# Kernel tuning notes

Hardware: AMD Instinct MI355X
Metric: run time of the kernel (lower is better)

## Reference

```python
import jax, jax.numpy as jnp
import numpy as np

N = 100000      # nodes
R = 3           # relations
E = 1600000     # edges per relation
IN, HID, OUT = 128, 128, 64


def setup_inputs() -> dict:
    key = jax.random.key(0)
    ks = jax.random.split(key, 16)
    x = jax.random.normal(ks[0], (N, IN), dtype=jnp.float32)
    src = jax.random.randint(ks[1], (R, E), 0, N, dtype=jnp.int32)
    dst = jax.random.randint(ks[2], (R, E), 0, N, dtype=jnp.int32)
    dims = [(IN, HID), (HID, HID), (HID, HID), (HID, HID), (HID, HID), (HID, OUT)]
    inp = {"x": x, "src": src, "dst": dst}
    for i, (di, do) in enumerate(dims):
        w = jax.random.normal(ks[3 + i], (R, di, do), dtype=jnp.float32) / np.sqrt(di).astype(np.float32)
        inp[f"W{i+1}"] = w
        inp[f"b{i+1}"] = jnp.zeros((R, do), dtype=jnp.float32)
    return inp


def _degree_norms(src, dst):
    # GraphConv norm='both': scale by out-deg(src)^-1/2 before, in-deg(dst)^-1/2 after
    ones = jnp.ones((E,), dtype=jnp.float32)
    inv_out, inv_in = [], []
    for r in range(R):
        d_out = jax.ops.segment_sum(ones, src[r], num_segments=N)
        d_in = jax.ops.segment_sum(ones, dst[r], num_segments=N)
        inv_out.append(jax.lax.rsqrt(jnp.maximum(d_out, 1.0))[:, None])
        inv_in.append(jax.lax.rsqrt(jnp.maximum(d_in, 1.0))[:, None])
    return inv_out, inv_in


def _hetero_conv(h, W, b, src, dst, inv_out, inv_in):
    # sum over relations of GraphConv_r(h): D_dst^-1/2 A_r (D_src^-1/2 h) W_r + b_r
    out = None
    for r in range(R):
        m = (h * inv_out[r]) @ W[r]                      # [N, do], weight-first (same math)
        agg = jax.ops.segment_sum(m[src[r]], dst[r], num_segments=N)
        term = agg * inv_in[r] + b[r]
        out = term if out is None else out + term
    return out


def reference(x, src, dst, W1, b1, W2, b2, W3, b3, W4, b4, W5, b5, W6, b6):
    inv_out, inv_in = _degree_norms(src, dst)
    h = x
    for W, b in [(W1, b1), (W2, b2), (W3, b3), (W4, b4), (W5, b5)]:
        h = jax.nn.relu(_hetero_conv(h, W, b, src, dst, inv_out, inv_in))
    return _hetero_conv(h, W6, b6, src, dst, inv_out, inv_in)
```

## Files before the change

kernel.cpp:

```cpp
#include <hip/hip_runtime.h>
#include <hip/hip_bf16.h>
#include <hip/hip_fp16.h>

constexpr int N_NODES = 100000;
constexpr int N_REL   = 3;
constexpr int N_EDGE  = 1600000;
constexpr int NCHUNK  = (N_NODES + 1023) / 1024;

constexpr int CCHUNK = 50;
constexpr int CH     = N_EDGE / CCHUNK;
constexpr int SUBN   = 50000;
constexpr int WPP    = SUBN / 4;
constexpr int CWORDS = N_NODES / 4;

constexpr int BSH  = 7;
constexpr int BNPB = 1 << BSH;
constexpr int NB   = (N_NODES + BNPB - 1) / BNPB;

typedef __attribute__((ext_vector_type(8))) short short8;
typedef __attribute__((ext_vector_type(4))) float f32x4;

__device__ inline ushort f2bf(float x) {
  unsigned u = __float_as_uint(x);
  unsigned r = u + 0x7FFFu + ((u >> 16) & 1u);
  return (ushort)(r >> 16);
}
__device__ inline float bf2f(ushort h) { return __uint_as_float(((unsigned)h) << 16); }


__global__ __launch_bounds__(1024)
void count_kernel(const int* __restrict__ src, const int* __restrict__ dst,
                  uint* __restrict__ part) {
  int c = blockIdx.x, r = blockIdx.y, dir = blockIdx.z;
  const int* ids = (dir ? dst : src) + (size_t)r * N_EDGE + (size_t)c * CH;
  uint* p = part + ((size_t)(c * N_REL + r) * 2 + dir) * CWORDS;
  __shared__ uint hist[WPP];
  #pragma unroll
  for (int pass = 0; pass < 2; pass++) {
    int base = pass * SUBN;
    for (int i = threadIdx.x; i < WPP; i += 1024) hist[i] = 0u;
    __syncthreads();
    for (int e = (int)threadIdx.x; e < CH; e += 1024) {
      int ln = ids[e] - base;
      if ((unsigned)ln < (unsigned)SUBN)
        atomicAdd(&hist[ln >> 2], 1u << ((ln & 3) * 8));
    }
    __syncthreads();
    for (int i = threadIdx.x; i < WPP; i += 1024) p[pass * WPP + i] = hist[i];
    __syncthreads();
  }
}

__global__ void reduce_kernel(const uint* __restrict__ part,
                              int* __restrict__ deg_out, int* __restrict__ deg_in) {
  int i = blockIdx.x * 256 + threadIdx.x;
  if (i >= N_REL * CWORDS) return;
  int r = i / CWORDS, w = i % CWORDS;
  uint aoe = 0, aoo = 0, aie = 0, aio = 0;
  for (int c = 0; c < CCHUNK; c++) {
    uint vo = part[((size_t)(c * N_REL + r) * 2 + 0) * CWORDS + w];
    uint vi = part[((size_t)(c * N_REL + r) * 2 + 1) * CWORDS + w];
    aoe += vo & 0x00FF00FFu; aoo += (vo >> 8) & 0x00FF00FFu;
    aie += vi & 0x00FF00FFu; aio += (vi >> 8) & 0x00FF00FFu;
  }
  int4 dout = make_int4((int)(aoe & 0xFFFFu), (int)(aoo & 0xFFFFu),
                        (int)(aoe >> 16),     (int)(aoo >> 16));
  int4 din  = make_int4((int)(aie & 0xFFFFu), (int)(aio & 0xFFFFu),
                        (int)(aie >> 16),     (int)(aio >> 16));
  *(int4*)&deg_out[(size_t)r * N_NODES + w * 4] = dout;
  *(int4*)&deg_in [(size_t)r * N_NODES + w * 4] = din;
}

__global__ void inv_kernel(const int* __restrict__ deg_out, const int* __restrict__ deg_in,
                           float* __restrict__ inv_out, float* __restrict__ inv_in) {
  int i = blockIdx.x * blockDim.x + threadIdx.x;
  if (i >= N_REL * N_NODES) return;
  inv_out[i] = rsqrtf(fmaxf((float)deg_out[i], 1.0f));
  inv_in[i]  = rsqrtf(fmaxf((float)deg_in[i],  1.0f));
}

__global__ void scan1_kernel(const int* __restrict__ deg_in, int* __restrict__ excl,
                             int* __restrict__ part) {
  int r = blockIdx.y;
  int i = blockIdx.x * 1024 + threadIdx.x;
  int v = (i < N_NODES) ? deg_in[r * N_NODES + i] : 0;
  __shared__ int sm[1024];
  sm[threadIdx.x] = v;
  __syncthreads();
  for (int off = 1; off < 1024; off <<= 1) {
    int t = (threadIdx.x >= (unsigned)off) ? sm[threadIdx.x - off] : 0;
    __syncthreads();
    sm[threadIdx.x] += t;
    __syncthreads();
  }
  if (i < N_NODES) excl[r * N_NODES + i] = sm[threadIdx.x] - v;
  if (threadIdx.x == 1023) part[r * NCHUNK + blockIdx.x] = sm[1023];
}

__global__ void scan2_kernel(int* __restrict__ part) {
  int r = blockIdx.x;
  int* p = part + r * NCHUNK;
  __shared__ int sm[128];
  int tid = threadIdx.x;
  int v = (tid < NCHUNK) ? p[tid] : 0;
  sm[tid] = v;
  __syncthreads();
  for (int off = 1; off < 128; off <<= 1) {
    int t = (tid >= off) ? sm[tid - off] : 0;
    __syncthreads();
    sm[tid] += t;
    __syncthreads();
  }
  if (tid < NCHUNK) p[tid] = sm[tid] - v;
}

__global__ void scan3_kernel(const int* __restrict__ excl, const int* __restrict__ part,
                             int* __restrict__ row_off) {
  int r = blockIdx.y;
  int i = blockIdx.x * 1024 + threadIdx.x;
  if (i < N_NODES) row_off[r * (N_NODES + 1) + i] = excl[r * N_NODES + i] + part[r * NCHUNK + (i >> 10)];
  if (i == N_NODES) row_off[r * (N_NODES + 1) + N_NODES] = N_EDGE;
}


__global__ __launch_bounds__(64)
void boff_kernel(const uint* __restrict__ cpart, int* __restrict__ boff) {
  int b = blockIdx.x, r = blockIdx.y;
  int lane = threadIdx.x;
  __shared__ int cnt_l[CCHUNK];
  for (int c = 0; c < CCHUNK; c++) {
    int w = b * 32 + (lane & 31);
    uint v = 0;
    if (w < CWORDS)
      v = cpart[((size_t)(c * N_REL + r) * 2 + 1) * CWORDS + w];
    int s = (int)((v & 0xFFu) + ((v >> 8) & 0xFFu) + ((v >> 16) & 0xFFu) + (v >> 24));
    #pragma unroll
    for (int k = 16; k >= 1; k >>= 1) s += __shfl_xor(s, k);
    if (lane == 0) cnt_l[c] = s;
  }
  __syncthreads();
  if (lane == 0) {
    int run = 0;
    for (int c = 0; c < CCHUNK; c++) { int t = cnt_l[c]; cnt_l[c] = run; run += t; }
  }
  __syncthreads();
  for (int c = lane; c < CCHUNK; c += 64)
    boff[((size_t)c * N_REL + r) * NB + c * 0 + b] = cnt_l[c];
}

__global__ __launch_bounds__(1024)
void bin2_kernel(const int* __restrict__ src, const int* __restrict__ dst,
                 const int* __restrict__ row_off, const int* __restrict__ boff,
                 int2* __restrict__ binned) {
  int c = blockIdx.x, r = blockIdx.y;
  __shared__ int cur[NB];
  for (int j = threadIdx.x; j < NB; j += 1024)
    cur[j] = row_off[r * (N_NODES + 1) + (j << BSH)] + boff[((size_t)c * N_REL + r) * NB + j];
  __syncthreads();
  const int* sp = src + (size_t)r * N_EDGE + (size_t)c * CH;
  const int* dp = dst + (size_t)r * N_EDGE + (size_t)c * CH;
  int2* bp = binned + (size_t)r * N_EDGE;
  for (int e = (int)threadIdx.x; e < CH; e += 1024) {
    int s = sp[e], d = dp[e];
    int slot = atomicAdd(&cur[d >> BSH], 1);
    bp[slot] = make_int2(s, d);
  }
}

__global__ __launch_bounds__(256)
void scatter2_kernel(const int2* __restrict__ binned, const int* __restrict__ row_off,
                     const float* __restrict__ inv_out, const float* __restrict__ inv_in,
                     float2* __restrict__ sorted_sc) {
  int b = blockIdx.x, r = blockIdx.y;
  int node0 = b << BSH;
  int node1 = min(node0 + BNPB, N_NODES);
  const int* ro = row_off + r * (N_NODES + 1);
  int base = ro[node0];
  int m    = ro[node1] - base;
  __shared__ int cur[BNPB];
  for (int j = threadIdx.x; j < node1 - node0; j += 256)
    cur[j] = ro[node0 + j] - base;
  __syncthreads();
  const int2* bp = binned + (size_t)r * N_EDGE + base;
  float2* op = sorted_sc + (size_t)r * N_EDGE + base;
  const float* ivo = inv_out + r * N_NODES;
  const float* ivi = inv_in  + r * N_NODES;
  for (int i = threadIdx.x; i < m; i += 256) {
    int2 rec = bp[i];
    int pos = atomicAdd(&cur[rec.y - node0], 1);
    float coef = ivo[rec.x] * ivi[rec.y];
    op[pos] = make_float2(__int_as_float(rec.x), coef);
  }
}

__global__ void convw_kernel(const float* __restrict__ W, ushort* __restrict__ Wh,
                             ushort* __restrict__ Wl, int DOv) {
  int idx = blockIdx.x * 256 + threadIdx.x;
  if (idx >= 384 * DOv) return;
  int k = idx / DOv, c = idx % DOv;
  float v = W[idx];
  ushort hh = f2bf(v);
  Wh[c * 384 + k] = hh;
  Wl[c * 384 + k] = f2bf(v - bf2f(hh));
}

__global__ void convx_kernel(const float* __restrict__ x, ushort* __restrict__ x16) {
  int i = blockIdx.x * 256 + threadIdx.x;
  if (i >= N_NODES * 32) return;
  f32x4 v = ((const f32x4*)x)[i];
  __half2 h0 = __floats2half2_rn(v.x, v.y);
  __half2 h1 = __floats2half2_rn(v.z, v.w);
  uint2 o;
  o.x = *(const unsigned*)&h0;
  o.y = *(const unsigned*)&h1;
  ((uint2*)x16)[i] = o;
}


template<int P>
__device__ inline void agg_pairs(const float2* __restrict__ scp, const uint2* __restrict__ hp,
                                 int e, int sub, int l32, f32x4& acc) {
  float2 q[P];
  #pragma unroll
  for (int j = 0; j < P; j++) q[j] = scp[e + 2 * j + sub];
  uint2 v[P];
  #pragma unroll
  for (int j = 0; j < P; j++) v[j] = hp[(size_t)__float_as_int(q[j].x) * 32 + l32];
  #pragma unroll
  for (int j = 0; j < P; j++) {
    __half2 h0 = *(const __half2*)&v[j].x;
    __half2 h1 = *(const __half2*)&v[j].y;
    float2 f0 = __half22float2(h0);
    float2 f1 = __half22float2(h1);
    acc.x = fmaf(q[j].y, f0.x, acc.x);
    acc.y = fmaf(q[j].y, f0.y, acc.y);
    acc.z = fmaf(q[j].y, f1.x, acc.z);
    acc.w = fmaf(q[j].y, f1.y, acc.w);
  }
}

__launch_bounds__(256)
__global__ void agg_kernel(const ushort* __restrict__ h, const float2* __restrict__ sc,
                           const int* __restrict__ row_off,
                           ushort* __restrict__ agg_hi, ushort* __restrict__ agg_lo) {
  int r    = blockIdx.y;
  int node = blockIdx.x * 4 + ((int)threadIdx.x >> 6);
  int lane = (int)threadIdx.x & 63;
  int sub  = lane >> 5;
  int l32  = lane & 31;
  if (node >= N_NODES) return;
  const int* ro = row_off + r * (N_NODES + 1);
  int beg = ro[node], end = ro[node + 1];
  const float2* scp = sc + (size_t)r * N_EDGE;
  const uint2* hp = (const uint2*)h;
  f32x4 acc = (f32x4){0.f, 0.f, 0.f, 0.f};
  int e = beg;
  while (e + 16 <= end) { agg_pairs<8>(scp, hp, e, sub, l32, acc); e += 16; }
  if (e + 8 <= end)     { agg_pairs<4>(scp, hp, e, sub, l32, acc); e += 8; }
  if (e + 4 <= end)     { agg_pairs<2>(scp, hp, e, sub, l32, acc); e += 4; }
  if (e + 2 <= end)     { agg_pairs<1>(scp, hp, e, sub, l32, acc); e += 2; }
  if (e < end && sub == 0) {
    float2 q = scp[e];
    uint2 v = hp[(size_t)__float_as_int(q.x) * 32 + l32];
    __half2 h0 = *(const __half2*)&v.x;
    __half2 h1 = *(const __half2*)&v.y;
    float2 f0 = __half22float2(h0);
    float2 f1 = __half22float2(h1);
    acc.x = fmaf(q.y, f0.x, acc.x);
    acc.y = fmaf(q.y, f0.y, acc.y);
    acc.z = fmaf(q.y, f1.x, acc.z);
    acc.w = fmaf(q.y, f1.y, acc.w);
  }
  acc.x += __shfl_xor(acc.x, 32);
  acc.y += __shfl_xor(acc.y, 32);
  acc.z += __shfl_xor(acc.z, 32);
  acc.w += __shfl_xor(acc.w, 32);
  float a0 = (sub == 0) ? acc.x : acc.z;
  float a1 = (sub == 0) ? acc.y : acc.w;
  ushort2 hi, lo;
  hi.x = f2bf(a0); lo.x = f2bf(a0 - bf2f(hi.x));
  hi.y = f2bf(a1); lo.y = f2bf(a1 - bf2f(hi.y));
  size_t base = (size_t)node * 384 + r * 128 + l32 * 4 + sub * 2;
  *(ushort2*)(agg_hi + base) = hi;
  *(ushort2*)(agg_lo + base) = lo;
}

template<int DO, bool F16OUT>
__launch_bounds__(256)
__global__ void gemm_kernel(const ushort* __restrict__ Ah, const ushort* __restrict__ Al,
                            const ushort* __restrict__ Wh, const ushort* __restrict__ Wl,
                            const float* __restrict__ b, float* __restrict__ out,
                            ushort* __restrict__ out16, int apply_relu) {
  constexpr int K   = 384;
  constexpr int KC  = 32;
  constexpr int NCT = DO / 16;
  constexpr int LDA = 40;
  __shared__ ushort As_hi[128 * LDA], As_lo[128 * LDA];
  __shared__ ushort Bs_hi[DO * LDA],  Bs_lo[DO * LDA];
  int tid  = threadIdx.x;
  int wave = tid >> 6, lane = tid & 63;
  int quad = lane >> 4, m16 = lane & 15;
  int m0 = blockIdx.x * 128;

  f32x4 acc[2][NCT];
  #pragma unroll
  for (int rt = 0; rt < 2; rt++)
    #pragma unroll
    for (int ct = 0; ct < NCT; ct++) acc[rt][ct] = (f32x4){0.f, 0.f, 0.f, 0.f};

  for (int kc = 0; kc < K; kc += KC) {
    __syncthreads();
    #pragma unroll
    for (int it = 0; it < 2; it++) {
      int idx = it * 256 + tid;
      int row = idx >> 2, kq = (idx & 3) * 8;
      uint4 vh = make_uint4(0u, 0u, 0u, 0u), vl = make_uint4(0u, 0u, 0u, 0u);
      if (m0 + row < N_NODES) {
        vh = *(const uint4*)(Ah + (size_t)(m0 + row) * K + kc + kq);
        vl = *(const uint4*)(Al + (size_t)(m0 + row) * K + kc + kq);
      }
      *(uint4*)&As_hi[row * LDA + kq] = vh;
      *(uint4*)&As_lo[row * LDA + kq] = vl;
    }
    #pragma unroll
    for (int it = 0; it < DO / 64; it++) {
      int idx = it * 256 + tid;
      int n = idx >> 2, kq = (idx & 3) * 8;
      *(uint4*)&Bs_hi[n * LDA + kq] = *(const uint4*)(Wh + (size_t)n * K + kc + kq);
      *(uint4*)&Bs_lo[n * LDA + kq] = *(const uint4*)(Wl + (size_t)n * K + kc + kq);
    }
    __syncthreads();

    short8 ah[2], al[2];
    #pragma unroll
    for (int rt = 0; rt < 2; rt++) {
      int m = wave * 32 + rt * 16 + m16;
      ah[rt] = *(const short8*)&As_hi[m * LDA + quad * 8];
      al[rt] = *(const short8*)&As_lo[m * LDA + quad * 8];
    }
    #pragma unroll
    for (int ct = 0; ct < NCT; ct++) {
      int n = ct * 16 + m16;
      short8 bh = *(const short8*)&Bs_hi[n * LDA + quad * 8];
      short8 bl = *(const short8*)&Bs_lo[n * LDA + quad * 8];
      #pragma unroll
      for (int rt = 0; rt < 2; rt++) {
        acc[rt][ct] = __builtin_amdgcn_mfma_f32_16x16x32_bf16(ah[rt], bh, acc[rt][ct], 0, 0, 0);
        acc[rt][ct] = __builtin_amdgcn_mfma_f32_16x16x32_bf16(ah[rt], bl, acc[rt][ct], 0, 0, 0);
        acc[rt][ct] = __builtin_amdgcn_mfma_f32_16x16x32_bf16(al[rt], bh, acc[rt][ct], 0, 0, 0);
      }
    }
  }
  #pragma unroll
  for (int ct = 0; ct < NCT; ct++) {
    int col = ct * 16 + m16;
    float bs = b[col] + b[DO + col] + b[2 * DO + col];
    #pragma unroll
    for (int rt = 0; rt < 2; rt++) {
      #pragma unroll
      for (int v = 0; v < 4; v++) {
        int row = m0 + wave * 32 + rt * 16 + quad * 4 + v;
        if (row < N_NODES) {
          float o = acc[rt][ct][v] + bs;
          if (apply_relu) o = fmaxf(o, 0.f);
          if (F16OUT) {
            __half ho = __float2half_rn(o);
            out16[(size_t)row * DO + col] = *(const ushort*)&ho;
          } else {
            out[(size_t)row * DO + col] = o;
          }
        }
      }
    }
  }
}


extern "C" void kernel_launch(void* const* d_in, const int* in_sizes, int n_in,
                              void* d_out, int out_size, void* d_ws, size_t ws_size,
                              hipStream_t stream) {
  const float* x   = (const float*)d_in[0];
  const int*   src = (const int*)d_in[1];
  const int*   dst = (const int*)d_in[2];
  const float* Wl6[6]; const float* bl[6];
  for (int i = 0; i < 6; i++) { Wl6[i] = (const float*)d_in[3 + 2*i]; bl[i] = (const float*)d_in[4 + 2*i]; }

  char* ws = (char*)d_ws;
  size_t off = 0;
  auto take = [&](size_t bytes) -> char* {
    char* p = ws + off;
    off = (off + bytes + 255) & ~(size_t)255;
    return p;
  };
  ushort* h16     = (ushort*)take((size_t)N_NODES * 128 * 2);
  ushort* agg_hi  = (ushort*)take((size_t)N_NODES * 384 * 2);
  ushort* agg_lo  = (ushort*)take((size_t)N_NODES * 384 * 2);
  int*    deg     = (int*)  take((size_t)2 * N_REL * N_NODES * 4);
  int*    deg_out = deg;
  int*    deg_in  = deg + N_REL * N_NODES;
  float*  inv_out = (float*)take((size_t)N_REL * N_NODES * 4);
  float*  inv_in  = (float*)take((size_t)N_REL * N_NODES * 4);
  int*    row_off = (int*)  take((size_t)N_REL * (N_NODES + 1) * 4);
  int*    part    = (int*)  take((size_t)N_REL * NCHUNK * 4);
  int*    boff    = (int*)  take((size_t)CCHUNK * N_REL * NB * 4);
  float2* s_sc    = (float2*)take((size_t)N_REL * N_EDGE * 8);
  ushort* Wt      = (ushort*)take((size_t)6 * 384 * 128 * 2 * 2);
  int*    excl    = (int*)agg_hi;
  int2*   binned  = (int2*)((char*)agg_hi + (size_t)(2 << 20));
  uint*   cpart   = (uint*)agg_lo;
  (void)ws_size; (void)in_sizes; (void)n_in; (void)out_size;

  const int nblocks = (N_REL * N_NODES + 255) / 256;

  count_kernel<<<dim3(CCHUNK, N_REL, 2), 1024, 0, stream>>>(src, dst, cpart);
  reduce_kernel<<<(N_REL * CWORDS + 255) / 256, 256, 0, stream>>>(cpart, deg_out, deg_in);
  inv_kernel<<<nblocks, 256, 0, stream>>>(deg_out, deg_in, inv_out, inv_in);
  scan1_kernel<<<dim3(NCHUNK, 3), 1024, 0, stream>>>(deg_in, excl, part);
  scan2_kernel<<<3, 128, 0, stream>>>(part);
  scan3_kernel<<<dim3(NCHUNK + 1, 3), 1024, 0, stream>>>(excl, part, row_off);
  boff_kernel<<<dim3(NB, N_REL), 64, 0, stream>>>(cpart, boff);
  bin2_kernel<<<dim3(CCHUNK, N_REL), 1024, 0, stream>>>(src, dst, row_off, boff, binned);
  scatter2_kernel<<<dim3(NB, N_REL), 256, 0, stream>>>(binned, row_off, inv_out, inv_in, s_sc);

  convx_kernel<<<(N_NODES * 32 + 255) / 256, 256, 0, stream>>>(x, h16);

  ushort* Wh[6]; ushort* Wlo[6];
  {
    size_t woff = 0;
    for (int L = 0; L < 6; L++) {
      int DOv = (L < 5) ? 128 : 64;
      Wh[L]  = Wt + woff;  woff += (size_t)384 * DOv;
      Wlo[L] = Wt + woff;  woff += (size_t)384 * DOv;
      convw_kernel<<<(384 * DOv + 255) / 256, 256, 0, stream>>>(Wl6[L], Wh[L], Wlo[L], DOv);
    }
  }

  const int mtiles = (N_NODES + 127) / 128;
  const int agg_blocks = (N_NODES + 3) / 4;
  for (int L = 0; L < 6; L++) {
    agg_kernel<<<dim3(agg_blocks, 3), 256, 0, stream>>>(h16, s_sc, row_off, agg_hi, agg_lo);
    if (L < 5) {
      gemm_kernel<128, true><<<mtiles, 256, 0, stream>>>(agg_hi, agg_lo, Wh[L], Wlo[L], bl[L],
                                                         nullptr, h16, 1);
    } else {
      gemm_kernel<64, false><<<mtiles, 256, 0, stream>>>(agg_hi, agg_lo, Wh[L], Wlo[L], bl[L],
                                                         (float*)d_out, nullptr, 0);
    }
  }
}
```

Baseline: 1.826 ms.

## Fuse neighbor aggregation into GEMM kernel with ping-pong feature buffers

Replaces the separate aggregation kernel and GEMM kernel with one fused kernel per layer. Each block of 64 nodes gathers neighbor features for each relation into swizzled shared memory, then immediately runs the split-bf16 MFMA against that relation's weight slice. This removes the round trip of the large hi/lo aggregate buffers through global memory. Because a layer now reads and writes node features in the same launch, it ping-pongs between two feature buffers. The trade-off is that each wave aggregates 16 nodes serially, and gather latency is no longer overlapped with MFMA work across separate kernels, which may lower occupancy and parallelism.

```diff
diff --git a/kernel.cpp b/kernel.cpp
--- a/kernel.cpp
+++ b/kernel.cpp
@@ -145,7 +145,7 @@
   }
   __syncthreads();
   for (int c = lane; c < CCHUNK; c += 64)
-    boff[((size_t)c * N_REL + r) * NB + c * 0 + b] = cnt_l[c];
+    boff[((size_t)c * N_REL + r) * NB + b] = cnt_l[c];
 }
 
 __global__ __launch_bounds__(1024)
@@ -239,136 +239,114 @@
   }
 }
 
-__launch_bounds__(256)
-__global__ void agg_kernel(const ushort* __restrict__ h, const float2* __restrict__ sc,
-                           const int* __restrict__ row_off,
-                           ushort* __restrict__ agg_hi, ushort* __restrict__ agg_lo) {
-  int r    = blockIdx.y;
-  int node = blockIdx.x * 4 + ((int)threadIdx.x >> 6);
-  int lane = (int)threadIdx.x & 63;
-  int sub  = lane >> 5;
-  int l32  = lane & 31;
-  if (node >= N_NODES) return;
-  const int* ro = row_off + r * (N_NODES + 1);
-  int beg = ro[node], end = ro[node + 1];
-  const float2* scp = sc + (size_t)r * N_EDGE;
-  const uint2* hp = (const uint2*)h;
-  f32x4 acc = (f32x4){0.f, 0.f, 0.f, 0.f};
-  int e = beg;
-  while (e + 16 <= end) { agg_pairs<8>(scp, hp, e, sub, l32, acc); e += 16; }
-  if (e + 8 <= end)     { agg_pairs<4>(scp, hp, e, sub, l32, acc); e += 8; }
-  if (e + 4 <= end)     { agg_pairs<2>(scp, hp, e, sub, l32, acc); e += 4; }
-  if (e + 2 <= end)     { agg_pairs<1>(scp, hp, e, sub, l32, acc); e += 2; }
-  if (e < end && sub == 0) {
-    float2 q = scp[e];
-    uint2 v = hp[(size_t)__float_as_int(q.x) * 32 + l32];
-    __half2 h0 = *(const __half2*)&v.x;
-    __half2 h1 = *(const __half2*)&v.y;
-    float2 f0 = __half22float2(h0);
-    float2 f1 = __half22float2(h1);
-    acc.x = fmaf(q.y, f0.x, acc.x);
-    acc.y = fmaf(q.y, f0.y, acc.y);
-    acc.z = fmaf(q.y, f1.x, acc.z);
-    acc.w = fmaf(q.y, f1.y, acc.w);
-  }
-  acc.x += __shfl_xor(acc.x, 32);
-  acc.y += __shfl_xor(acc.y, 32);
-  acc.z += __shfl_xor(acc.z, 32);
-  acc.w += __shfl_xor(acc.w, 32);
-  float a0 = (sub == 0) ? acc.x : acc.z;
-  float a1 = (sub == 0) ? acc.y : acc.w;
-  ushort2 hi, lo;
-  hi.x = f2bf(a0); lo.x = f2bf(a0 - bf2f(hi.x));
-  hi.y = f2bf(a1); lo.y = f2bf(a1 - bf2f(hi.y));
-  size_t base = (size_t)node * 384 + r * 128 + l32 * 4 + sub * 2;
-  *(ushort2*)(agg_hi + base) = hi;
-  *(ushort2*)(agg_lo + base) = lo;
-}
-
 template<int DO, bool F16OUT>
 __launch_bounds__(256)
-__global__ void gemm_kernel(const ushort* __restrict__ Ah, const ushort* __restrict__ Al,
-                            const ushort* __restrict__ Wh, const ushort* __restrict__ Wl,
-                            const float* __restrict__ b, float* __restrict__ out,
-                            ushort* __restrict__ out16, int apply_relu) {
-  constexpr int K   = 384;
-  constexpr int KC  = 32;
+__global__ void fused_kernel(const ushort* __restrict__ h, const float2* __restrict__ sc,
+                             const int* __restrict__ row_off,
+                             const ushort* __restrict__ Wh, const ushort* __restrict__ Wl,
+                             const float* __restrict__ b, float* __restrict__ out,
+                             ushort* __restrict__ out16, int apply_relu) {
   constexpr int NCT = DO / 16;
-  constexpr int LDA = 40;
-  __shared__ ushort As_hi[128 * LDA], As_lo[128 * LDA];
-  __shared__ ushort Bs_hi[DO * LDA],  Bs_lo[DO * LDA];
+  __shared__ ushort As_hi[64 * 128], As_lo[64 * 128];
+  __shared__ ushort Bs_hi[DO * 32],  Bs_lo[DO * 32];
   int tid  = threadIdx.x;
   int wave = tid >> 6, lane = tid & 63;
+  int sub  = lane >> 5, l32 = lane & 31;
   int quad = lane >> 4, m16 = lane & 15;
-  int m0 = blockIdx.x * 128;
-
-  f32x4 acc[2][NCT];
-  #pragma unroll
-  for (int rt = 0; rt < 2; rt++)
-    #pragma unroll
-    for (int ct = 0; ct < NCT; ct++) acc[rt][ct] = (f32x4){0.f, 0.f, 0.f, 0.f};
-
-  for (int kc = 0; kc < K; kc += KC) {
-    __syncthreads();
-    #pragma unroll
-    for (int it = 0; it < 2; it++) {
-      int idx = it * 256 + tid;
-      int row = idx >> 2, kq = (idx & 3) * 8;
-      uint4 vh = make_uint4(0u, 0u, 0u, 0u), vl = make_uint4(0u, 0u, 0u, 0u);
-      if (m0 + row < N_NODES) {
-        vh = *(const uint4*)(Ah + (size_t)(m0 + row) * K + kc + kq);
-        vl = *(const uint4*)(Al + (size_t)(m0 + row) * K + kc + kq);
+  int n0 = blockIdx.x * 64;
+  const uint2* hp = (const uint2*)h;
+
+  f32x4 acc[NCT];
+  #pragma unroll
+  for (int ct = 0; ct < NCT; ct++) acc[ct] = (f32x4){0.f, 0.f, 0.f, 0.f};
+
+  for (int r = 0; r < N_REL; r++) {
+    const int* ro = row_off + r * (N_NODES + 1);
+    const float2* scp = sc + (size_t)r * N_EDGE;
+    for (int t = 0; t < 16; t++) {
+      int row  = wave * 16 + t;
+      int node = n0 + row;
+      f32x4 a = (f32x4){0.f, 0.f, 0.f, 0.f};
+      if (node < N_NODES) {
+        int beg = ro[node], end = ro[node + 1];
+        int e = beg;
+        while (e + 16 <= end) { agg_pairs<8>(scp, hp, e, sub, l32, a); e += 16; }
+        if (e + 8 <= end)     { agg_pairs<4>(scp, hp, e, sub, l32, a); e += 8; }
+        if (e + 4 <= end)     { agg_pairs<2>(scp, hp, e, sub, l32, a); e += 4; }
+        if (e + 2 <= end)     { agg_pairs<1>(scp, hp, e, sub, l32, a); e += 2; }
+        if (e < end && sub == 0) {
+          float2 q = scp[e];
+          uint2 v = hp[(size_t)__float_as_int(q.x) * 32 + l32];
+          __half2 h0 = *(const __half2*)&v.x;
+          __half2 h1 = *(const __half2*)&v.y;
+          float2 f0 = __half22float2(h0);
+          float2 f1 = __half22float2(h1);
+          a.x = fmaf(q.y, f0.x, a.x);
+          a.y = fmaf(q.y, f0.y, a.y);
+          a.z = fmaf(q.y, f1.x, a.z);
+          a.w = fmaf(q.y, f1.y, a.w);
+        }
       }
-      *(uint4*)&As_hi[row * LDA + kq] = vh;
-      *(uint4*)&As_lo[row * LDA + kq] = vl;
-    }
-    #pragma unroll
-    for (int it = 0; it < DO / 64; it++) {
-      int idx = it * 256 + tid;
-      int n = idx >> 2, kq = (idx & 3) * 8;
-      *(uint4*)&Bs_hi[n * LDA + kq] = *(const uint4*)(Wh + (size_t)n * K + kc + kq);
-      *(uint4*)&Bs_lo[n * LDA + kq] = *(const uint4*)(Wl + (size_t)n * K + kc + kq);
-    }
-    __syncthreads();
-
-    short8 ah[2], al[2];
-    #pragma unroll
-    for (int rt = 0; rt < 2; rt++) {
-      int m = wave * 32 + rt * 16 + m16;
-      ah[rt] = *(const short8*)&As_hi[m * LDA + quad * 8];
-      al[rt] = *(const short8*)&As_lo[m * LDA + quad * 8];
-    }
-    #pragma unroll
-    for (int ct = 0; ct < NCT; ct++) {
-      int n = ct * 16 + m16;
-      short8 bh = *(const short8*)&Bs_hi[n * LDA + quad * 8];
-      short8 bl = *(const short8*)&Bs_lo[n * LDA + quad * 8];
+      a.x += __shfl_xor(a.x, 32);
+      a.y += __shfl_xor(a.y, 32);
+      a.z += __shfl_xor(a.z, 32);
+      a.w += __shfl_xor(a.w, 32);
+      float a0 = (sub == 0) ? a.x : a.z;
+      float a1 = (sub == 0) ? a.y : a.w;
+      ushort2 hi, lo;
+      hi.x = f2bf(a0); lo.x = f2bf(a0 - bf2f(hi.x));
+      hi.y = f2bf(a1); lo.y = f2bf(a1 - bf2f(hi.y));
+      int col = l32 * 4 + sub * 2;
+      int idx = (row * 128 + col) ^ ((row & 7) << 3);
+      *(ushort2*)&As_hi[idx] = hi;
+      *(ushort2*)&As_lo[idx] = lo;
+    }
+
+    for (int kc = 0; kc < 128; kc += 32) {
+      __syncthreads();
       #pragma unroll
-      for (int rt = 0; rt < 2; rt++) {
-        acc[rt][ct] = __builtin_amdgcn_mfma_f32_16x16x32_bf16(ah[rt], bh, acc[rt][ct], 0, 0, 0);
-        acc[rt][ct] = __builtin_amdgcn_mfma_f32_16x16x32_bf16(ah[rt], bl, acc[rt][ct], 0, 0, 0);
-        acc[rt][ct] = __builtin_amdgcn_mfma_f32_16x16x32_bf16(al[rt], bh, acc[rt][ct], 0, 0, 0);
+      for (int it = 0; it < DO / 64; it++) {
+        int idx = it * 256 + tid;
+        int n = idx >> 2, kq = (idx & 3) * 8;
+        int bi = (n * 32 + kq) ^ ((n & 7) << 3);
+        *(uint4*)&Bs_hi[bi] = *(const uint4*)(Wh + (size_t)n * 384 + r * 128 + kc + kq);
+        *(uint4*)&Bs_lo[bi] = *(const uint4*)(Wl + (size_t)n * 384 + r * 128 + kc + kq);
       }
-    }
-  }
+      __syncthreads();
+
+      int arow = wave * 16 + m16;
+      int ai = (arow * 128 + kc + quad * 8) ^ ((arow & 7) << 3);
+      short8 ah = *(const short8*)&As_hi[ai];
+      short8 al = *(const short8*)&As_lo[ai];
+      #pragma unroll
+      for (int ct = 0; ct < NCT; ct++) {
+        int n = ct * 16 + m16;
+        int bi = (n * 32 + quad * 8) ^ ((n & 7) << 3);
+        short8 bh = *(const short8*)&Bs_hi[bi];
+        short8 bl = *(const short8*)&Bs_lo[bi];
+        acc[ct] = __builtin_amdgcn_mfma_f32_16x16x32_bf16(ah, bh, acc[ct], 0, 0, 0);
+        acc[ct] = __builtin_amdgcn_mfma_f32_16x16x32_bf16(ah, bl, acc[ct], 0, 0, 0);
+        acc[ct] = __builtin_amdgcn_mfma_f32_16x16x32_bf16(al, bh, acc[ct], 0, 0, 0);
+      }
+    }
+    __syncthreads();
+  }
+
   #pragma unroll
   for (int ct = 0; ct < NCT; ct++) {
     int col = ct * 16 + m16;
     float bs = b[col] + b[DO + col] + b[2 * DO + col];
     #pragma unroll
-    for (int rt = 0; rt < 2; rt++) {
-      #pragma unroll
-      for (int v = 0; v < 4; v++) {
-        int row = m0 + wave * 32 + rt * 16 + quad * 4 + v;
-        if (row < N_NODES) {
-          float o = acc[rt][ct][v] + bs;
-          if (apply_relu) o = fmaxf(o, 0.f);
-          if (F16OUT) {
-            __half ho = __float2half_rn(o);
-            out16[(size_t)row * DO + col] = *(const ushort*)&ho;
-          } else {
-            out[(size_t)row * DO + col] = o;
-          }
+    for (int v = 0; v < 4; v++) {
+      int row = n0 + wave * 16 + quad * 4 + v;
+      if (row < N_NODES) {
+        float o = acc[ct][v] + bs;
+        if (apply_relu) o = fmaxf(o, 0.f);
+        if (F16OUT) {
+          __half ho = __float2half_rn(o);
+          out16[(size_t)row * DO + col] = *(const ushort*)&ho;
+        } else {
+          out[(size_t)row * DO + col] = o;
         }
       }
     }
@@ -392,9 +370,8 @@
     off = (off + bytes + 255) & ~(size_t)255;
     return p;
   };
-  ushort* h16     = (ushort*)take((size_t)N_NODES * 128 * 2);
-  ushort* agg_hi  = (ushort*)take((size_t)N_NODES * 384 * 2);
-  ushort* agg_lo  = (ushort*)take((size_t)N_NODES * 384 * 2);
+  ushort* h16a    = (ushort*)take((size_t)N_NODES * 128 * 2);
+  ushort* h16b    = (ushort*)take((size_t)N_NODES * 128 * 2);
   int*    deg     = (int*)  take((size_t)2 * N_REL * N_NODES * 4);
   int*    deg_out = deg;
   int*    deg_in  = deg + N_REL * N_NODES;
@@ -405,9 +382,9 @@
   int*    boff    = (int*)  take((size_t)CCHUNK * N_REL * NB * 4);
   float2* s_sc    = (float2*)take((size_t)N_REL * N_EDGE * 8);
   ushort* Wt      = (ushort*)take((size_t)6 * 384 * 128 * 2 * 2);
-  int*    excl    = (int*)agg_hi;
-  int2*   binned  = (int2*)((char*)agg_hi + (size_t)(2 << 20));
-  uint*   cpart   = (uint*)agg_lo;
+  int*    excl    = (int*)  take((size_t)N_REL * N_NODES * 4);
+  uint*   cpart   = (uint*) take((size_t)CCHUNK * N_REL * 2 * CWORDS * 4);
+  int2*   binned  = (int2*) take((size_t)N_REL * N_EDGE * 8);
   (void)ws_size; (void)in_sizes; (void)n_in; (void)out_size;
 
   const int nblocks = (N_REL * N_NODES + 255) / 256;
@@ -422,7 +399,7 @@
   bin2_kernel<<<dim3(CCHUNK, N_REL), 1024, 0, stream>>>(src, dst, row_off, boff, binned);
   scatter2_kernel<<<dim3(NB, N_REL), 256, 0, stream>>>(binned, row_off, inv_out, inv_in, s_sc);
 
-  convx_kernel<<<(N_NODES * 32 + 255) / 256, 256, 0, stream>>>(x, h16);
+  convx_kernel<<<(N_NODES * 32 + 255) / 256, 256, 0, stream>>>(x, h16a);
 
   ushort* Wh[6]; ushort* Wlo[6];
   {
@@ -435,16 +412,19 @@
     }
   }
 
-  const int mtiles = (N_NODES + 127) / 128;
-  const int agg_blocks = (N_NODES + 3) / 4;
+  const int mtiles = (N_NODES + 63) / 64;
+  ushort* hin  = h16a;
+  ushort* hout = h16b;
   for (int L = 0; L < 6; L++) {
-    agg_kernel<<<dim3(agg_blocks, 3), 256, 0, stream>>>(h16, s_sc, row_off, agg_hi, agg_lo);
     if (L < 5) {
-      gemm_kernel<128, true><<<mtiles, 256, 0, stream>>>(agg_hi, agg_lo, Wh[L], Wlo[L], bl[L],
-                                                         nullptr, h16, 1);
+      fused_kernel<128, true><<<mtiles, 256, 0, stream>>>(hin, s_sc, row_off,
+                                                          Wh[L], Wlo[L], bl[L],
+                                                          nullptr, hout, 1);
+      ushort* t = hin; hin = hout; hout = t;
     } else {
-      gemm_kernel<64, false><<<mtiles, 256, 0, stream>>>(agg_hi, agg_lo, Wh[L], Wlo[L], bl[L],
-                                                         (float*)d_out, nullptr, 0);
-    }
-  }
-}
+      fused_kernel<64, false><<<mtiles, 256, 0, stream>>>(hin, s_sc, row_off,
+                                                          Wh[L], Wlo[L], bl[L],
+                                                          (float*)d_out, nullptr, 0);
+    }
+  }
+}
```

Result: slower. 2.566 ms (+40.5%).
